# Performance work log

Measured on AMD Instinct MI355X. Metric: run time of the kernel, lower is better.

## Reference

```python
import jax, jax.numpy as jnp
import numpy as np

NUM_USERS = 100000
NUM_PRODUCTS = 50000
USER_FEAT_DIM = 128
PROD_FEAT_DIM = 128
EMBED_DIM = 256
NUM_EDGES = 250000
N_NODES = NUM_USERS + NUM_PRODUCTS


def gcn_conv(x, src, dst, W, b, n_nodes):
    """PyG GCNConv: symmetric normalization with added self-loops, then linear.
    x: [N, Din]; src/dst: [E] directed edges (message src -> dst); W: [Din, Dout]."""
    h = x @ W  # [N, Dout]
    loop = jnp.arange(n_nodes, dtype=src.dtype)
    s = jnp.concatenate([src, loop])
    d = jnp.concatenate([dst, loop])
    deg = jax.ops.segment_sum(jnp.ones(s.shape[0], dtype=h.dtype), d, num_segments=n_nodes)
    dinv = jax.lax.rsqrt(jnp.maximum(deg, 1.0))  # deg >= 1 thanks to self-loops
    norm = dinv[s] * dinv[d]  # [E+N]
    msg = h[s] * norm[:, None]  # [E+N, Dout]
    out = jax.ops.segment_sum(msg, d, num_segments=n_nodes)
    return out + b


def setup_inputs() -> dict:
    key = jax.random.key(0)
    ks = jax.random.split(key, 20)
    D = EMBED_DIM
    u_idx = jax.random.randint(ks[0], (NUM_EDGES,), 0, NUM_USERS)
    p_idx = jax.random.randint(ks[1], (NUM_EDGES,), NUM_USERS, NUM_USERS + NUM_PRODUCTS)
    edge_index = jnp.stack([u_idx, p_idx], axis=0)  # [2, E]

    def lin(k, fan_in, shape):
        bound = 1.0 / np.sqrt(fan_in)
        return jax.random.uniform(k, shape, jnp.float32, -bound, bound)

    return {
        "edge_index": edge_index,
        "user_features": jax.random.normal(ks[2], (NUM_USERS, USER_FEAT_DIM), jnp.float32),
        "product_features": jax.random.normal(ks[3], (NUM_PRODUCTS, PROD_FEAT_DIM), jnp.float32),
        "user_emb": jax.random.normal(ks[4], (NUM_USERS, D), jnp.float32),
        "prod_emb": jax.random.normal(ks[5], (NUM_PRODUCTS, D), jnp.float32),
        "uW": lin(ks[6], USER_FEAT_DIM, (USER_FEAT_DIM, D)),
        "ub": lin(ks[7], USER_FEAT_DIM, (D,)),
        "pW": lin(ks[8], PROD_FEAT_DIM, (PROD_FEAT_DIM, D)),
        "pb": lin(ks[9], PROD_FEAT_DIM, (D,)),
        "c1W": lin(ks[10], D, (D, D)),
        "c1b": jnp.zeros((D,), jnp.float32),
        "c2W": lin(ks[11], D, (D, D)),
        "c2b": jnp.zeros((D,), jnp.float32),
        "m1W": lin(ks[12], 2 * D, (2 * D, D)),
        "m1b": lin(ks[13], 2 * D, (D,)),
        "m2W": lin(ks[14], D, (D, 1)),
        "m2b": lin(ks[15], D, (1,)),
    }


def reference(edge_index, user_features, product_features, user_emb, prod_emb,
              uW, ub, pW, pb, c1W, c1b, c2W, c2b, m1W, m1b, m2W, m2b):
    user_idx = edge_index[0]          # [E] in [0, NUM_USERS)
    prod_idx = edge_index[1]          # [E] in [NUM_USERS, N_NODES)
    prod_local = prod_idx - NUM_USERS

    # combined bidirectional edges: forward (u->p) and reverse (p->u)
    src = jnp.concatenate([user_idx, prod_idx])
    dst = jnp.concatenate([prod_idx, user_idx])

    # embedding + linear fusion
    user_x = user_features @ uW + ub + user_emb       # [NUM_USERS, D]
    prod_x = product_features @ pW + pb + prod_emb    # [NUM_PRODUCTS, D]
    x = jnp.concatenate([user_x, prod_x], axis=0)     # [N, D]

    x = jax.nn.relu(gcn_conv(x, src, dst, c1W, c1b, N_NODES))
    # dropout p=0.2 is identity in eval mode
    x = gcn_conv(x, src, dst, c2W, c2b, N_NODES)

    user_out = x[:NUM_USERS]
    prod_out = x[NUM_USERS:]
    pair = jnp.concatenate([user_out[user_idx], prod_out[prod_local]], axis=1)  # [E, 2D]
    h = jax.nn.relu(pair @ m1W + m1b)
    preds = (h @ m2W + m2b).squeeze(-1)  # [E]
    return preds
```

## Files before the change

kernel.cpp:

```cpp
#include <hip/hip_runtime.h>
#include <hip/hip_bf16.h>
#include <cstdint>

#define NUM_USERS 100000
#define NUM_PRODUCTS 50000
#define N_NODES 150000
#define NUM_EDGES 250000
#define D 256

typedef __attribute__((ext_vector_type(8))) short bf16x8;
typedef __attribute__((ext_vector_type(4))) float f32x4;
typedef __attribute__((ext_vector_type(4))) unsigned short u16x4;

__device__ __forceinline__ unsigned short f2bf(float f) {
    union { float f; unsigned u; } x; x.f = f;
    unsigned r = x.u + 0x7fff + ((x.u >> 16) & 1);
    return (unsigned short)(r >> 16);
}
__device__ __forceinline__ float bf2f(unsigned short h) {
    union { unsigned u; float f; } x; x.u = ((unsigned)h) << 16;
    return x.f;
}

__global__ __launch_bounds__(256) void count_deg(const int* __restrict__ ei, int* __restrict__ cnt, int E) {
    int e = blockIdx.x * 256 + threadIdx.x;
    if (e < E) {
        atomicAdd(&cnt[ei[e]], 1);
        atomicAdd(&cnt[ei[E + e]], 1);
    }
}

__global__ __launch_bounds__(256) void compute_dinv(const int* __restrict__ cnt, float* __restrict__ dinv, int N) {
    int n = blockIdx.x * 256 + threadIdx.x;
    if (n < N) dinv[n] = rsqrtf((float)(cnt[n] + 1));
}

#define SCAN_CHUNK 1024

__global__ __launch_bounds__(256) void scan_partials(const int* __restrict__ cnt, int* __restrict__ bsum, int N) {
    __shared__ int sdata[256];
    int base = blockIdx.x * SCAN_CHUNK;
    int t = threadIdx.x;
    int s = 0;
#pragma unroll
    for (int i = 0; i < 4; i++) {
        int idx = base + t * 4 + i;
        if (idx < N) s += cnt[idx];
    }
    sdata[t] = s;
    __syncthreads();
    for (int off = 128; off > 0; off >>= 1) {
        if (t < off) sdata[t] += sdata[t + off];
        __syncthreads();
    }
    if (t == 0) bsum[blockIdx.x] = sdata[0];
}

__global__ __launch_bounds__(256) void scan_bsums(const int* __restrict__ bsum, int* __restrict__ bscan,
                                                  int NB, int* __restrict__ offs, int N) {
    __shared__ int s[256];
    int t = threadIdx.x;
    int v = (t < NB) ? bsum[t] : 0;
    s[t] = v;
    __syncthreads();
    for (int off = 1; off < 256; off <<= 1) {
        int x = (t >= off) ? s[t - off] : 0;
        __syncthreads();
        s[t] += x;
        __syncthreads();
    }
    if (t < NB) bscan[t] = s[t] - v;
    if (t == 255) offs[N] = s[255];
}

__global__ __launch_bounds__(256) void scan_final(const int* __restrict__ cnt, const int* __restrict__ bscan,
                                                  int* __restrict__ offs, int N) {
    __shared__ int sdata[256];
    int base = blockIdx.x * SCAN_CHUNK;
    int t = threadIdx.x;
    int v[4];
    int loc = 0;
#pragma unroll
    for (int i = 0; i < 4; i++) {
        int idx = base + t * 4 + i;
        v[i] = (idx < N) ? cnt[idx] : 0;
        loc += v[i];
    }
    int mine = loc;
    sdata[t] = loc;
    __syncthreads();
    for (int off = 1; off < 256; off <<= 1) {
        int x = (t >= off) ? sdata[t - off] : 0;
        __syncthreads();
        sdata[t] += x;
        __syncthreads();
    }
    int pre = sdata[t] - mine + bscan[blockIdx.x];
#pragma unroll
    for (int i = 0; i < 4; i++) {
        int idx = base + t * 4 + i;
        if (idx < N) offs[idx] = pre;
        pre += v[i];
    }
}

__global__ __launch_bounds__(256) void fill_adj(const int* __restrict__ ei, const int* __restrict__ offs,
                                                int* __restrict__ cursor, int* __restrict__ adj, int E) {
    int e = blockIdx.x * 256 + threadIdx.x;
    if (e >= E) return;
    int u = ei[e];
    int p = ei[E + e];
    int pos = atomicAdd(&cursor[u], 1);
    adj[offs[u] + pos] = p;
    pos = atomicAdd(&cursor[p], 1);
    adj[offs[p] + pos] = u;
}

__global__ __launch_bounds__(256) void convW(const float* __restrict__ W, unsigned short* __restrict__ Wth,
                                             unsigned short* __restrict__ Wtl, int K) {
    int n = threadIdx.x;
    int k = blockIdx.x;
    float v = W[(size_t)k * 256 + n];
    unsigned short h = f2bf(v);
    Wth[(size_t)n * K + k] = h;
    Wtl[(size_t)n * K + k] = f2bf(v - bf2f(h));
}

__global__ __launch_bounds__(256) void splitF(const float* __restrict__ in, unsigned short* __restrict__ h,
                                              unsigned short* __restrict__ l, int n4) {
    int i = blockIdx.x * 256 + threadIdx.x;
    if (i >= n4) return;
    f32x4 v = *(const f32x4*)(in + (size_t)i * 4);
    u16x4 hv, lv;
#pragma unroll
    for (int j = 0; j < 4; j++) {
        unsigned short hh = f2bf(v[j]);
        hv[j] = hh;
        lv[j] = f2bf(v[j] - bf2f(hh));
    }
    *(u16x4*)(h + (size_t)i * 4) = hv;
    *(u16x4*)(l + (size_t)i * 4) = lv;
}

__device__ __forceinline__ void stage_tile(const unsigned short* __restrict__ plane, int row0, int rclamp,
                                           int ldK, int koff, char* ldsbase, int t) {
#pragma unroll
    for (int i = 0; i < 4; i++) {
        int chunk = i * 256 + t;
        int r = chunk >> 3;
        int c = chunk & 7;
        int grow = row0 + r;
        if (grow > rclamp) grow = rclamp;
        const unsigned short* src = plane + (size_t)grow * ldK + koff + ((c ^ (r & 7)) << 3);
        __builtin_amdgcn_global_load_lds((const __attribute__((address_space(1))) unsigned int*)src,
                                         (__attribute__((address_space(3))) unsigned int*)(ldsbase + chunk * 16),
                                         16, 0, 0);
    }
}

template <int K, int MODE>
__global__ __launch_bounds__(256, 2) void gemm_mfma(
    const unsigned short* __restrict__ Ah, const unsigned short* __restrict__ Al,
    const unsigned short* __restrict__ Bh, const unsigned short* __restrict__ Bl,
    const float* __restrict__ bias, const float* __restrict__ addv,
    const float* __restrict__ scale,
    float* __restrict__ outF,
    unsigned short* __restrict__ outH, unsigned short* __restrict__ outL,
    int Mrows, int out_base) {
    __shared__ char lds[65536];
    const int t = threadIdx.x;
    const int lane = t & 63;
    const int wid = t >> 6;
    const int wr = wid >> 1, wc = wid & 1;
    const int row0 = blockIdx.x * 128;
    const int col0 = blockIdx.y * 128;
    const int l15 = lane & 15;
    const int l4 = lane >> 4;

    char* ldsAh = lds;
    char* ldsAl = lds + 16384;
    char* ldsBh = lds + 32768;
    char* ldsBl = lds + 49152;

    f32x4 acc[4][4];
#pragma unroll
    for (int i = 0; i < 4; i++)
#pragma unroll
        for (int j = 0; j < 4; j++)
#pragma unroll
            for (int q = 0; q < 4; q++) acc[i][j][q] = 0.f;

    for (int ks = 0; ks < K / 64; ks++) {
        if (ks) __syncthreads();
        int koff = ks * 64;
        stage_tile(Ah, row0, Mrows - 1, K, koff, ldsAh, t);
        stage_tile(Al, row0, Mrows - 1, K, koff, ldsAl, t);
        stage_tile(Bh, col0, 255, K, koff, ldsBh, t);
        stage_tile(Bl, col0, 255, K, koff, ldsBl, t);
        asm volatile("s_waitcnt vmcnt(0)" ::: "memory");
        __syncthreads();
#pragma unroll
        for (int kk = 0; kk < 2; kk++) {
            int kc = kk * 4 + l4;
            bf16x8 ah[4], al[4], bh[4], bl[4];
#pragma unroll
            for (int mf = 0; mf < 4; mf++) {
                int r = wr * 64 + mf * 16 + l15;
                int pc = (kc ^ (r & 7)) << 4;
                ah[mf] = *(const bf16x8*)(ldsAh + r * 128 + pc);
                al[mf] = *(const bf16x8*)(ldsAl + r * 128 + pc);
            }
#pragma unroll
            for (int nf = 0; nf < 4; nf++) {
                int r = wc * 64 + nf * 16 + l15;
                int pc = (kc ^ (r & 7)) << 4;
                bh[nf] = *(const bf16x8*)(ldsBh + r * 128 + pc);
                bl[nf] = *(const bf16x8*)(ldsBl + r * 128 + pc);
            }
#pragma unroll
            for (int mf = 0; mf < 4; mf++)
#pragma unroll
                for (int nf = 0; nf < 4; nf++) {
                    acc[mf][nf] = __builtin_amdgcn_mfma_f32_16x16x32_bf16(ah[mf], bh[nf], acc[mf][nf], 0, 0, 0);
                    acc[mf][nf] = __builtin_amdgcn_mfma_f32_16x16x32_bf16(ah[mf], bl[nf], acc[mf][nf], 0, 0, 0);
                    acc[mf][nf] = __builtin_amdgcn_mfma_f32_16x16x32_bf16(al[mf], bh[nf], acc[mf][nf], 0, 0, 0);
                }
        }
    }

    __syncthreads();
    float* ldsC = (float*)lds;
#pragma unroll
    for (int mf = 0; mf < 4; mf++)
#pragma unroll
        for (int nf = 0; nf < 4; nf++) {
            int r = wr * 64 + mf * 16 + l4 * 4;
            int c = wc * 64 + nf * 16 + l15;
#pragma unroll
            for (int j = 0; j < 4; j++) ldsC[(r + j) * 128 + c] = acc[mf][nf][j];
        }
    __syncthreads();

    const int cg = t & 31;
    const int r0 = t >> 5;
#pragma unroll
    for (int i = 0; i < 16; i++) {
        int r = r0 + i * 8;
        int grow = row0 + r;
        if (grow >= Mrows) continue;
        f32x4 v = *(const f32x4*)&ldsC[r * 128 + cg * 4];
        int gc = col0 + cg * 4;
        if (MODE == 1) {
            f32x4 bv = *(const f32x4*)(bias + gc);
            f32x4 av = *(const f32x4*)(addv + (size_t)grow * 256 + gc);
            v += bv + av;
        } else if (MODE == 2) {
            v *= scale[grow];
        }
        size_t ob = (size_t)(out_base + grow) * 256 + gc;
        if (MODE == 1) {
            u16x4 hv, lv;
#pragma unroll
            for (int j = 0; j < 4; j++) {
                unsigned short h = f2bf(v[j]);
                hv[j] = h;
                lv[j] = f2bf(v[j] - bf2f(h));
            }
            *(u16x4*)(outH + ob) = hv;
            *(u16x4*)(outL + ob) = lv;
        } else {
            *(f32x4*)(outF + ob) = v;
        }
    }
}

__global__ __launch_bounds__(256) void gcn_aggregate_f32(
    const float* __restrict__ g, const int* __restrict__ offs, const int* __restrict__ adj,
    const float* __restrict__ dinv, const float* __restrict__ bias,
    unsigned short* __restrict__ xh, unsigned short* __restrict__ xl, int do_relu) {
    int wave = threadIdx.x >> 6;
    int lane = threadIdx.x & 63;
    int d = blockIdx.x * 4 + wave;
    int c0 = lane * 4;

    f32x4 acc0 = *(const f32x4*)&g[(size_t)d * D + c0];
    f32x4 acc1 = {0.f, 0.f, 0.f, 0.f};
    int beg = offs[d], end = offs[d + 1];
    int i = beg;
    for (; i + 1 < end; i += 2) {
        int s0 = adj[i];
        int s1 = adj[i + 1];
        f32x4 v0 = *(const f32x4*)&g[(size_t)s0 * D + c0];
        f32x4 v1 = *(const f32x4*)&g[(size_t)s1 * D + c0];
        acc0 += v0;
        acc1 += v1;
    }
    if (i < end) {
        int s = adj[i];
        acc0 += *(const f32x4*)&g[(size_t)s * D + c0];
    }
    f32x4 acc = acc0 + acc1;

    float dv = dinv[d];
    f32x4 bv = *(const f32x4*)&bias[c0];
    u16x4 hv, lv;
#pragma unroll
    for (int j = 0; j < 4; j++) {
        float v = fmaf(dv, acc[j], bv[j]);
        if (do_relu) v = fmaxf(v, 0.f);
        unsigned short h = f2bf(v);
        hv[j] = h;
        lv[j] = f2bf(v - bf2f(h));
    }
    size_t ob = (size_t)d * D + c0;
    *(u16x4*)(xh + ob) = hv;
    *(u16x4*)(xl + ob) = lv;
}

__global__ __launch_bounds__(256) void edge_mlp(
    const float* __restrict__ ab, const int* __restrict__ ei,
    const float* __restrict__ m1b, const float* __restrict__ m2w, const float* __restrict__ m2b,
    float* __restrict__ preds, int E) {
    int wave = threadIdx.x >> 6;
    int lane = threadIdx.x & 63;
    int e = blockIdx.x * 4 + wave;
    if (e >= E) return;
    int u = ei[e];
    int p = ei[E + e];
    int c0 = lane * 4;
    f32x4 au = *(const f32x4*)&ab[(size_t)u * D + c0];
    f32x4 bp = *(const f32x4*)&ab[(size_t)p * D + c0];
    f32x4 bb = *(const f32x4*)&m1b[c0];
    f32x4 w = *(const f32x4*)&m2w[c0];
    float h0 = fmaxf(au[0] + bp[0] + bb[0], 0.f);
    float h1 = fmaxf(au[1] + bp[1] + bb[1], 0.f);
    float h2 = fmaxf(au[2] + bp[2] + bb[2], 0.f);
    float h3 = fmaxf(au[3] + bp[3] + bb[3], 0.f);
    float partial = h0 * w[0] + h1 * w[1] + h2 * w[2] + h3 * w[3];
#pragma unroll
    for (int off = 32; off > 0; off >>= 1) partial += __shfl_down(partial, off);
    if (lane == 0) preds[e] = partial + m2b[0];
}

extern "C" void kernel_launch(void* const* d_in, const int* in_sizes, int n_in,
                              void* d_out, int out_size, void* d_ws, size_t ws_size,
                              hipStream_t stream) {
    const int* ei = (const int*)d_in[0];
    const float* user_feat = (const float*)d_in[1];
    const float* prod_feat = (const float*)d_in[2];
    const float* user_emb = (const float*)d_in[3];
    const float* prod_emb = (const float*)d_in[4];
    const float* uW = (const float*)d_in[5];
    const float* ub = (const float*)d_in[6];
    const float* pW = (const float*)d_in[7];
    const float* pb = (const float*)d_in[8];
    const float* c1W = (const float*)d_in[9];
    const float* c1b = (const float*)d_in[10];
    const float* c2W = (const float*)d_in[11];
    const float* c2b = (const float*)d_in[12];
    const float* m1W = (const float*)d_in[13];
    const float* m1b = (const float*)d_in[14];
    const float* m2w = (const float*)d_in[15];
    const float* m2b = (const float*)d_in[16];
    float* preds = (float*)d_out;

    uint8_t* ws = (uint8_t*)d_ws;
    size_t off = 0;
    auto alloc = [&](size_t bytes) {
        size_t o = off;
        off = (off + bytes + 255) & ~(size_t)255;
        return o;
    };
    const size_t NROW = (size_t)N_NODES * D;
    unsigned short* xh = (unsigned short*)(ws + alloc(NROW * 2));
    unsigned short* xl = (unsigned short*)(ws + alloc(NROW * 2));
    uint8_t* Greg = ws + alloc(NROW * 4);
    float* gF = (float*)Greg;
    float* ab = (float*)Greg;
    unsigned short* ufh = (unsigned short*)Greg;
    unsigned short* ufl = ufh + (size_t)NUM_USERS * 128;
    unsigned short* pfh = ufl + (size_t)NUM_USERS * 128;
    unsigned short* pfl = pfh + (size_t)NUM_PRODUCTS * 128;

    unsigned short* uWth = (unsigned short*)(ws + alloc(256 * 128 * 2));
    unsigned short* uWtl = (unsigned short*)(ws + alloc(256 * 128 * 2));
    unsigned short* pWth = (unsigned short*)(ws + alloc(256 * 128 * 2));
    unsigned short* pWtl = (unsigned short*)(ws + alloc(256 * 128 * 2));
    unsigned short* c1h = (unsigned short*)(ws + alloc(256 * 256 * 2));
    unsigned short* c1l = (unsigned short*)(ws + alloc(256 * 256 * 2));
    unsigned short* c2h = (unsigned short*)(ws + alloc(256 * 256 * 2));
    unsigned short* c2l = (unsigned short*)(ws + alloc(256 * 256 * 2));
    unsigned short* m1th = (unsigned short*)(ws + alloc(256 * 256 * 2));
    unsigned short* m1tl = (unsigned short*)(ws + alloc(256 * 256 * 2));
    unsigned short* m1bh = (unsigned short*)(ws + alloc(256 * 256 * 2));
    unsigned short* m1bl = (unsigned short*)(ws + alloc(256 * 256 * 2));

    float* dinv = (float*)(ws + alloc((size_t)N_NODES * 4));
    int* cnt = (int*)(ws + alloc((size_t)N_NODES * 4));
    int* cursor = (int*)(ws + alloc((size_t)N_NODES * 4));
    int* offs = (int*)(ws + alloc((size_t)(N_NODES + 1) * 4));
    int* adj = (int*)(ws + alloc((size_t)2 * NUM_EDGES * 4));
    int* bsum = (int*)(ws + alloc(4096));
    int* bscan = (int*)(ws + alloc(4096));

    const int NB = (N_NODES + SCAN_CHUNK - 1) / SCAN_CHUNK;

    hipMemsetAsync(cnt, 0, (size_t)N_NODES * 4, stream);
    hipMemsetAsync(cursor, 0, (size_t)N_NODES * 4, stream);

    count_deg<<<(NUM_EDGES + 255) / 256, 256, 0, stream>>>(ei, cnt, NUM_EDGES);
    compute_dinv<<<(N_NODES + 255) / 256, 256, 0, stream>>>(cnt, dinv, N_NODES);
    scan_partials<<<NB, 256, 0, stream>>>(cnt, bsum, N_NODES);
    scan_bsums<<<1, 256, 0, stream>>>(bsum, bscan, NB, offs, N_NODES);
    scan_final<<<NB, 256, 0, stream>>>(cnt, bscan, offs, N_NODES);
    fill_adj<<<(NUM_EDGES + 255) / 256, 256, 0, stream>>>(ei, offs, cursor, adj, NUM_EDGES);

    convW<<<128, 256, 0, stream>>>(uW, uWth, uWtl, 128);
    convW<<<128, 256, 0, stream>>>(pW, pWth, pWtl, 128);
    convW<<<256, 256, 0, stream>>>(c1W, c1h, c1l, 256);
    convW<<<256, 256, 0, stream>>>(c2W, c2h, c2l, 256);
    convW<<<256, 256, 0, stream>>>(m1W, m1th, m1tl, 256);
    convW<<<256, 256, 0, stream>>>(m1W + 256 * 256, m1bh, m1bl, 256);

    splitF<<<(NUM_USERS * 128 / 4 + 255) / 256, 256, 0, stream>>>(user_feat, ufh, ufl, NUM_USERS * 128 / 4);
    splitF<<<(NUM_PRODUCTS * 128 / 4 + 255) / 256, 256, 0, stream>>>(prod_feat, pfh, pfl, NUM_PRODUCTS * 128 / 4);

    const int TU = (NUM_USERS + 127) / 128;
    const int TP = (NUM_PRODUCTS + 127) / 128;
    const int TN = (N_NODES + 127) / 128;

    gemm_mfma<128, 1><<<dim3(TU, 2), 256, 0, stream>>>(ufh, ufl, uWth, uWtl, ub, user_emb, nullptr,
                                                       nullptr, xh, xl, NUM_USERS, 0);
    gemm_mfma<128, 1><<<dim3(TP, 2), 256, 0, stream>>>(pfh, pfl, pWth, pWtl, pb, prod_emb, nullptr,
                                                       nullptr, xh, xl, NUM_PRODUCTS, NUM_USERS);

    gemm_mfma<256, 2><<<dim3(TN, 2), 256, 0, stream>>>(xh, xl, c1h, c1l, nullptr, nullptr, dinv,
                                                       gF, nullptr, nullptr, N_NODES, 0);
    gcn_aggregate_f32<<<N_NODES / 4, 256, 0, stream>>>(gF, offs, adj, dinv, c1b, xh, xl, 1);

    gemm_mfma<256, 2><<<dim3(TN, 2), 256, 0, stream>>>(xh, xl, c2h, c2l, nullptr, nullptr, dinv,
                                                       gF, nullptr, nullptr, N_NODES, 0);
    gcn_aggregate_f32<<<N_NODES / 4, 256, 0, stream>>>(gF, offs, adj, dinv, c2b, xh, xl, 0);

    gemm_mfma<256, 0><<<dim3(TU, 2), 256, 0, stream>>>(xh, xl, m1th, m1tl, nullptr, nullptr, nullptr,
                                                       ab, nullptr, nullptr, NUM_USERS, 0);
    gemm_mfma<256, 0><<<dim3(TP, 2), 256, 0, stream>>>(xh + (size_t)NUM_USERS * D, xl + (size_t)NUM_USERS * D,
                                                       m1bh, m1bl, nullptr, nullptr, nullptr,
                                                       ab, nullptr, nullptr, NUM_PRODUCTS, NUM_USERS);

    edge_mlp<<<NUM_EDGES / 4, 256, 0, stream>>>(ab, ei, m1b, m2w, m2b, preds, NUM_EDGES);
}
```

Measured before the change: 1.028 ms.

## Halve GEMM LDS via interleaved hi/lo K=32 tiles, raise occupancy; unroll aggregation

The split-bf16 GEMM now stages K=32 slices with the hi and lo planes interleaved in one swizzled LDS tile per operand. This halves shared memory to 32KB, and launch bounds are raised to allow three blocks per CU. The epilogue writes C through LDS in two 64-row halves so it fits the smaller buffer. The GCN aggregation loop is unrolled to four independent accumulators and uses nontemporal stores. The cost is twice as many barrier and stage iterations per K, and tighter register limits.

```diff
diff --git a/kernel.cpp b/kernel.cpp
--- a/kernel.cpp
+++ b/kernel.cpp
@@ -142,16 +142,21 @@
     *(u16x4*)(l + (size_t)i * 4) = lv;
 }
 
-__device__ __forceinline__ void stage_tile(const unsigned short* __restrict__ plane, int row0, int rclamp,
-                                           int ldK, int koff, char* ldsbase, int t) {
-#pragma unroll
-    for (int i = 0; i < 4; i++) {
-        int chunk = i * 256 + t;
+__device__ __forceinline__ void stage_tile32(const unsigned short* __restrict__ ph,
+                                             const unsigned short* __restrict__ pl,
+                                             int row0, int rclamp, int ldK, int koff,
+                                             char* ldsbase, int t) {
+#pragma unroll
+    for (int j = 0; j < 4; j++) {
+        int chunk = j * 256 + t;
         int r = chunk >> 3;
-        int c = chunk & 7;
+        int s = chunk & 7;
+        int u = s ^ (r & 7);
+        int kc = u & 3;
         int grow = row0 + r;
         if (grow > rclamp) grow = rclamp;
-        const unsigned short* src = plane + (size_t)grow * ldK + koff + ((c ^ (r & 7)) << 3);
+        const unsigned short* base = (u & 4) ? pl : ph;
+        const unsigned short* src = base + (size_t)grow * ldK + koff + kc * 8;
         __builtin_amdgcn_global_load_lds((const __attribute__((address_space(1))) unsigned int*)src,
                                          (__attribute__((address_space(3))) unsigned int*)(ldsbase + chunk * 16),
                                          16, 0, 0);
@@ -159,7 +164,7 @@
 }
 
 template <int K, int MODE>
-__global__ __launch_bounds__(256, 2) void gemm_mfma(
+__global__ __launch_bounds__(256, 3) void gemm_mfma(
     const unsigned short* __restrict__ Ah, const unsigned short* __restrict__ Al,
     const unsigned short* __restrict__ Bh, const unsigned short* __restrict__ Bl,
     const float* __restrict__ bias, const float* __restrict__ addv,
@@ -167,7 +172,7 @@
     float* __restrict__ outF,
     unsigned short* __restrict__ outH, unsigned short* __restrict__ outL,
     int Mrows, int out_base) {
-    __shared__ char lds[65536];
+    __shared__ char lds[32768];
     const int t = threadIdx.x;
     const int lane = t & 63;
     const int wid = t >> 6;
@@ -177,10 +182,8 @@
     const int l15 = lane & 15;
     const int l4 = lane >> 4;
 
-    char* ldsAh = lds;
-    char* ldsAl = lds + 16384;
-    char* ldsBh = lds + 32768;
-    char* ldsBl = lds + 49152;
+    char* ldsA = lds;
+    char* ldsB = lds + 16384;
 
     f32x4 acc[4][4];
 #pragma unroll
@@ -190,87 +193,83 @@
 #pragma unroll
             for (int q = 0; q < 4; q++) acc[i][j][q] = 0.f;
 
-    for (int ks = 0; ks < K / 64; ks++) {
+    for (int ks = 0; ks < K / 32; ks++) {
         if (ks) __syncthreads();
-        int koff = ks * 64;
-        stage_tile(Ah, row0, Mrows - 1, K, koff, ldsAh, t);
-        stage_tile(Al, row0, Mrows - 1, K, koff, ldsAl, t);
-        stage_tile(Bh, col0, 255, K, koff, ldsBh, t);
-        stage_tile(Bl, col0, 255, K, koff, ldsBl, t);
+        int koff = ks * 32;
+        stage_tile32(Ah, Al, row0, Mrows - 1, K, koff, ldsA, t);
+        stage_tile32(Bh, Bl, col0, 255, K, koff, ldsB, t);
         asm volatile("s_waitcnt vmcnt(0)" ::: "memory");
         __syncthreads();
-#pragma unroll
-        for (int kk = 0; kk < 2; kk++) {
-            int kc = kk * 4 + l4;
-            bf16x8 ah[4], al[4], bh[4], bl[4];
-#pragma unroll
-            for (int mf = 0; mf < 4; mf++) {
-                int r = wr * 64 + mf * 16 + l15;
-                int pc = (kc ^ (r & 7)) << 4;
-                ah[mf] = *(const bf16x8*)(ldsAh + r * 128 + pc);
-                al[mf] = *(const bf16x8*)(ldsAl + r * 128 + pc);
+
+        bf16x8 bh[4], bl[4];
+#pragma unroll
+        for (int nf = 0; nf < 4; nf++) {
+            int r = wc * 64 + nf * 16 + l15;
+            bh[nf] = *(const bf16x8*)(ldsB + r * 128 + ((l4 ^ (r & 7)) << 4));
+            bl[nf] = *(const bf16x8*)(ldsB + r * 128 + (((4 | l4) ^ (r & 7)) << 4));
+        }
+#pragma unroll
+        for (int mf = 0; mf < 4; mf++) {
+            int r = wr * 64 + mf * 16 + l15;
+            bf16x8 ah = *(const bf16x8*)(ldsA + r * 128 + ((l4 ^ (r & 7)) << 4));
+            bf16x8 al = *(const bf16x8*)(ldsA + r * 128 + (((4 | l4) ^ (r & 7)) << 4));
+#pragma unroll
+            for (int nf = 0; nf < 4; nf++) {
+                acc[mf][nf] = __builtin_amdgcn_mfma_f32_16x16x32_bf16(ah, bh[nf], acc[mf][nf], 0, 0, 0);
+                acc[mf][nf] = __builtin_amdgcn_mfma_f32_16x16x32_bf16(ah, bl[nf], acc[mf][nf], 0, 0, 0);
+                acc[mf][nf] = __builtin_amdgcn_mfma_f32_16x16x32_bf16(al, bh[nf], acc[mf][nf], 0, 0, 0);
             }
-#pragma unroll
-            for (int nf = 0; nf < 4; nf++) {
-                int r = wc * 64 + nf * 16 + l15;
-                int pc = (kc ^ (r & 7)) << 4;
-                bh[nf] = *(const bf16x8*)(ldsBh + r * 128 + pc);
-                bl[nf] = *(const bf16x8*)(ldsBl + r * 128 + pc);
-            }
+        }
+    }
+
+    __syncthreads();
+    float* ldsC = (float*)lds;
+    const int cg = t & 31;
+    const int r0 = t >> 5;
+#pragma unroll
+    for (int half = 0; half < 2; half++) {
+        if (wr == half) {
 #pragma unroll
             for (int mf = 0; mf < 4; mf++)
 #pragma unroll
                 for (int nf = 0; nf < 4; nf++) {
-                    acc[mf][nf] = __builtin_amdgcn_mfma_f32_16x16x32_bf16(ah[mf], bh[nf], acc[mf][nf], 0, 0, 0);
-                    acc[mf][nf] = __builtin_amdgcn_mfma_f32_16x16x32_bf16(ah[mf], bl[nf], acc[mf][nf], 0, 0, 0);
-                    acc[mf][nf] = __builtin_amdgcn_mfma_f32_16x16x32_bf16(al[mf], bh[nf], acc[mf][nf], 0, 0, 0);
+                    int lr = mf * 16 + l4 * 4;
+                    int c = wc * 64 + nf * 16 + l15;
+#pragma unroll
+                    for (int q = 0; q < 4; q++) ldsC[(lr + q) * 128 + c] = acc[mf][nf][q];
                 }
         }
-    }
-
-    __syncthreads();
-    float* ldsC = (float*)lds;
-#pragma unroll
-    for (int mf = 0; mf < 4; mf++)
-#pragma unroll
-        for (int nf = 0; nf < 4; nf++) {
-            int r = wr * 64 + mf * 16 + l4 * 4;
-            int c = wc * 64 + nf * 16 + l15;
-#pragma unroll
-            for (int j = 0; j < 4; j++) ldsC[(r + j) * 128 + c] = acc[mf][nf][j];
+        __syncthreads();
+#pragma unroll
+        for (int i = 0; i < 8; i++) {
+            int lr = r0 + i * 8;
+            int grow = row0 + half * 64 + lr;
+            if (grow >= Mrows) continue;
+            f32x4 v = *(const f32x4*)&ldsC[lr * 128 + cg * 4];
+            int gc = col0 + cg * 4;
+            if (MODE == 1) {
+                f32x4 bv = *(const f32x4*)(bias + gc);
+                f32x4 av = *(const f32x4*)(addv + (size_t)grow * 256 + gc);
+                v += bv + av;
+            } else if (MODE == 2) {
+                v *= scale[grow];
+            }
+            size_t ob = (size_t)(out_base + grow) * 256 + gc;
+            if (MODE == 1) {
+                u16x4 hv, lv;
+#pragma unroll
+                for (int j = 0; j < 4; j++) {
+                    unsigned short h = f2bf(v[j]);
+                    hv[j] = h;
+                    lv[j] = f2bf(v[j] - bf2f(h));
+                }
+                *(u16x4*)(outH + ob) = hv;
+                *(u16x4*)(outL + ob) = lv;
+            } else {
+                *(f32x4*)(outF + ob) = v;
+            }
         }
-    __syncthreads();
-
-    const int cg = t & 31;
-    const int r0 = t >> 5;
-#pragma unroll
-    for (int i = 0; i < 16; i++) {
-        int r = r0 + i * 8;
-        int grow = row0 + r;
-        if (grow >= Mrows) continue;
-        f32x4 v = *(const f32x4*)&ldsC[r * 128 + cg * 4];
-        int gc = col0 + cg * 4;
-        if (MODE == 1) {
-            f32x4 bv = *(const f32x4*)(bias + gc);
-            f32x4 av = *(const f32x4*)(addv + (size_t)grow * 256 + gc);
-            v += bv + av;
-        } else if (MODE == 2) {
-            v *= scale[grow];
-        }
-        size_t ob = (size_t)(out_base + grow) * 256 + gc;
-        if (MODE == 1) {
-            u16x4 hv, lv;
-#pragma unroll
-            for (int j = 0; j < 4; j++) {
-                unsigned short h = f2bf(v[j]);
-                hv[j] = h;
-                lv[j] = f2bf(v[j] - bf2f(h));
-            }
-            *(u16x4*)(outH + ob) = hv;
-            *(u16x4*)(outL + ob) = lv;
-        } else {
-            *(f32x4*)(outF + ob) = v;
-        }
+        __syncthreads();
     }
 }
 
@@ -285,36 +284,37 @@
 
     f32x4 acc0 = *(const f32x4*)&g[(size_t)d * D + c0];
     f32x4 acc1 = {0.f, 0.f, 0.f, 0.f};
+    f32x4 acc2 = {0.f, 0.f, 0.f, 0.f};
+    f32x4 acc3 = {0.f, 0.f, 0.f, 0.f};
     int beg = offs[d], end = offs[d + 1];
     int i = beg;
-    for (; i + 1 < end; i += 2) {
-        int s0 = adj[i];
-        int s1 = adj[i + 1];
-        f32x4 v0 = *(const f32x4*)&g[(size_t)s0 * D + c0];
-        f32x4 v1 = *(const f32x4*)&g[(size_t)s1 * D + c0];
-        acc0 += v0;
-        acc1 += v1;
-    }
-    if (i < end) {
+    for (; i + 3 < end; i += 4) {
+        int s0 = adj[i], s1 = adj[i + 1], s2 = adj[i + 2], s3 = adj[i + 3];
+        acc0 += *(const f32x4*)&g[(size_t)s0 * D + c0];
+        acc1 += *(const f32x4*)&g[(size_t)s1 * D + c0];
+        acc2 += *(const f32x4*)&g[(size_t)s2 * D + c0];
+        acc3 += *(const f32x4*)&g[(size_t)s3 * D + c0];
+    }
+    for (; i < end; ++i) {
         int s = adj[i];
         acc0 += *(const f32x4*)&g[(size_t)s * D + c0];
     }
-    f32x4 acc = acc0 + acc1;
+    f32x4 acc = (acc0 + acc1) + (acc2 + acc3);
 
     float dv = dinv[d];
     f32x4 bv = *(const f32x4*)&bias[c0];
-    u16x4 hv, lv;
+    union { u16x4 v; unsigned long long q; } hv, lv;
 #pragma unroll
     for (int j = 0; j < 4; j++) {
         float v = fmaf(dv, acc[j], bv[j]);
         if (do_relu) v = fmaxf(v, 0.f);
         unsigned short h = f2bf(v);
-        hv[j] = h;
-        lv[j] = f2bf(v - bf2f(h));
+        hv.v[j] = h;
+        lv.v[j] = f2bf(v - bf2f(h));
     }
     size_t ob = (size_t)d * D + c0;
-    *(u16x4*)(xh + ob) = hv;
-    *(u16x4*)(xl + ob) = lv;
+    __builtin_nontemporal_store(hv.q, (unsigned long long*)(xh + ob));
+    __builtin_nontemporal_store(lv.q, (unsigned long long*)(xl + ob));
 }
 
 __global__ __launch_bounds__(256) void edge_mlp(
```

Result: no change. 1.022 ms (-0.6%).
